# Kernel optimization log

Hardware: AMD Instinct MI355X
Metric: run time of the kernel (lower is better)

Reference implementation:

```python
import jax, jax.numpy as jnp
import numpy as np

NUM_HEADS = 16
THETA = 10000.0


def _rope(x, pos, theta):
    # x: [b, h, s, d_k] with d_k even; rotate interleaved pairs (even, odd)
    d = x.shape[-1]
    inv_freq = theta ** (-jnp.arange(0, d, 2, dtype=jnp.float32) / d)  # [d/2]
    ang = pos.astype(jnp.float32)[:, None] * inv_freq                  # [s, d/2]
    cos = jnp.cos(ang)[None, None]                                     # [1,1,s,d/2]
    sin = jnp.sin(ang)[None, None]
    x1 = x[..., 0::2]
    x2 = x[..., 1::2]
    r1 = x1 * cos - x2 * sin
    r2 = x1 * sin + x2 * cos
    return jnp.stack([r1, r2], axis=-1).reshape(x.shape)


def setup_inputs() -> dict:
    key = jax.random.key(0)
    ks = jax.random.split(key, 5)
    B, S, D = 2, 2048, 1024
    x = jax.random.normal(ks[0], (B, S, D), dtype=jnp.float32)
    scale = 0.02
    Wq = jax.random.normal(ks[1], (D, D), dtype=jnp.float32) * scale
    Wk = jax.random.normal(ks[2], (D, D), dtype=jnp.float32) * scale
    Wv = jax.random.normal(ks[3], (D, D), dtype=jnp.float32) * scale
    Wo = jax.random.normal(ks[4], (D, D), dtype=jnp.float32) * scale
    return {"x": x, "Wq": Wq, "Wk": Wk, "Wv": Wv, "Wo": Wo}


def reference(x, Wq, Wk, Wv, Wo):
    B, S, D = x.shape
    H = NUM_HEADS
    dk = D // H
    # QKV projections (bias-free Linear: y = x @ W^T, W is [out, in])
    q = (x @ Wq.T).reshape(B, S, H, dk).transpose(0, 2, 1, 3)  # [b,h,s,dk]
    k = (x @ Wk.T).reshape(B, S, H, dk).transpose(0, 2, 1, 3)
    v = (x @ Wv.T).reshape(B, S, H, dk).transpose(0, 2, 1, 3)
    pos = jnp.arange(S)
    q = _rope(q, pos, THETA)
    k = _rope(k, pos, THETA)
    # naive masked SDPA, causal mask
    scores = jnp.einsum('bhqd,bhkd->bhqk', q, k) / (dk ** 0.5)
    causal = jnp.tril(jnp.ones((S, S), dtype=bool))
    scores = jnp.where(causal, scores, -jnp.inf)
    attn = jax.nn.softmax(scores, axis=-1)
    out = jnp.einsum('bhqk,bhkd->bhqd', attn, v)
    out = out.transpose(0, 2, 1, 3).reshape(B, S, D)
    return out @ Wo.T
```

## Files before the change

### kernel.cpp

```cpp
#include <hip/hip_runtime.h>
#include <hip/hip_bf16.h>
#include <stdint.h>

typedef __bf16 bf16;
typedef __bf16 bf16x8 __attribute__((ext_vector_type(8)));
typedef float f32x4 __attribute__((ext_vector_type(4)));

#define B_ 2
#define S_ 2048
#define D_ 1024
#define H_ 16
#define DK 64
#define M_ 4096

__device__ __forceinline__ void gload_lds16(const void* g, void* l) {
  __builtin_amdgcn_global_load_lds(
      (const __attribute__((address_space(1))) uint32_t*)(uintptr_t)g,
      (__attribute__((address_space(3))) uint32_t*)(uintptr_t)l, 16, 0, 0);
}

struct alignas(8) B4s { bf16 a, b, c, d; };

__global__ __launch_bounds__(256) void cvt_all_kernel(
    const float* __restrict__ x, const float* __restrict__ wq, const float* __restrict__ wk,
    const float* __restrict__ wv, const float* __restrict__ wo,
    bf16* __restrict__ xb, bf16* __restrict__ wqb, bf16* __restrict__ wkb,
    bf16* __restrict__ wvb, bf16* __restrict__ wob) {
  int i = blockIdx.x * 256 + threadIdx.x;
  const float* src;
  bf16* dst;
  int off;
  if (i < 1048576) { src = x; dst = xb; off = i; }
  else if (i < 1310720) { src = wq; dst = wqb; off = i - 1048576; }
  else if (i < 1572864) { src = wk; dst = wkb; off = i - 1310720; }
  else if (i < 1835008) { src = wv; dst = wvb; off = i - 1572864; }
  else { src = wo; dst = wob; off = i - 1835008; }
  float4 v = reinterpret_cast<const float4*>(src)[off];
  B4s o{(bf16)v.x, (bf16)v.y, (bf16)v.z, (bf16)v.w};
  reinterpret_cast<B4s*>(dst)[off] = o;
}

template <int MODE>
__global__ __launch_bounds__(256) void gemm_kernel(
    const bf16* __restrict__ A,
    const bf16* __restrict__ W0, const bf16* __restrict__ W1, const bf16* __restrict__ W2,
    bf16* __restrict__ q_out, bf16* __restrict__ k_out, bf16* __restrict__ v_out,
    float* __restrict__ c_out) {
  constexpr int BK = 32;
  __shared__ bf16 Alds[128 * BK];
  __shared__ bf16 Blds[128 * BK];
  const int tid = threadIdx.x;
  const int w = tid >> 6, l = tid & 63;
  const int lr = l & 15, lg = l >> 4;
  const int m0 = blockIdx.y * 128;
  const int nt = blockIdx.x;
  const bf16* W;
  int n0;
  if (MODE == 0) {
    W = (nt >> 3) == 0 ? W0 : ((nt >> 3) == 1 ? W1 : W2);
    n0 = (nt & 7) * 128;
  } else {
    W = W0;
    n0 = nt * 128;
  }
  const int K = 1024;
  const int wm = (w >> 1) * 64, wn = (w & 1) * 64;
  const int srow = w * 16 + (l >> 2);
  const int scol = (l & 3) * 8;
  f32x4 acc[4][4] = {};
  for (int k0 = 0; k0 < K; k0 += BK) {
    gload_lds16(A + (size_t)(m0 + srow) * K + k0 + scol, Alds + (w * 16) * BK);
    gload_lds16(A + (size_t)(m0 + 64 + srow) * K + k0 + scol, Alds + (64 + w * 16) * BK);
    gload_lds16(W + (size_t)(n0 + srow) * K + k0 + scol, Blds + (w * 16) * BK);
    gload_lds16(W + (size_t)(n0 + 64 + srow) * K + k0 + scol, Blds + (64 + w * 16) * BK);
    __syncthreads();
    bf16x8 af[4], bfr[4];
#pragma unroll
    for (int f = 0; f < 4; ++f) {
      af[f]  = *reinterpret_cast<const bf16x8*>(Alds + (wm + f * 16 + lr) * BK + lg * 8);
      bfr[f] = *reinterpret_cast<const bf16x8*>(Blds + (wn + f * 16 + lr) * BK + lg * 8);
    }
#pragma unroll
    for (int fm = 0; fm < 4; ++fm)
#pragma unroll
      for (int fn = 0; fn < 4; ++fn)
        acc[fm][fn] = __builtin_amdgcn_mfma_f32_16x16x32_bf16(af[fm], bfr[fn], acc[fm][fn], 0, 0, 0);
    __syncthreads();
  }
#pragma unroll
  for (int fm = 0; fm < 4; ++fm)
#pragma unroll
    for (int fn = 0; fn < 4; ++fn)
#pragma unroll
      for (int r = 0; r < 4; ++r) {
        int m = m0 + wm + fm * 16 + lg * 4 + r;
        int n = n0 + wn + fn * 16 + lr;
        float v = acc[fm][fn][r];
        if (MODE == 0) {
          bf16* dst = (nt >> 3) == 0 ? q_out : ((nt >> 3) == 1 ? k_out : v_out);
          int h = n >> 6, d = n & 63;
          int b = m >> 11, s = m & 2047;
          dst[(((size_t)b * H_ + h) * S_ + s) * DK + d] = (bf16)v;
        } else {
          c_out[(size_t)m * D_ + n] = v;
        }
      }
}

__global__ __launch_bounds__(256) void rope_kernel(bf16* __restrict__ Q, bf16* __restrict__ K) {
  const int NG = 32 * 2048 * 8;
  int idx = blockIdx.x * 256 + threadIdx.x;
  bf16* X = Q;
  float sc = 0.18033688f;
  if (idx >= NG) { X = K; idx -= NG; sc = 1.0f; }
  int g = idx & 7;
  int s = (idx >> 3) & 2047;
  int bh = idx >> 14;
  size_t off = ((size_t)bh * S_ + s) * DK + g * 8;
  bf16x8 v = *reinterpret_cast<const bf16x8*>(X + off);
  bf16x8 o;
  const float c0 = -0.4152410118609203f;
  float fs = (float)s;
#pragma unroll
  for (int p = 0; p < 4; ++p) {
    int i = g * 4 + p;
    float ang = fs * exp2f((float)i * c0);
    float sn = __sinf(ang), cs = __cosf(ang);
    float x1 = (float)v[2 * p], x2 = (float)v[2 * p + 1];
    o[2 * p]     = (bf16)((x1 * cs - x2 * sn) * sc);
    o[2 * p + 1] = (bf16)((x1 * sn + x2 * cs) * sc);
  }
  *reinterpret_cast<bf16x8*>(X + off) = o;
}

__global__ __launch_bounds__(256, 4) void attn_kernel(
    const bf16* __restrict__ Q, const bf16* __restrict__ K, const bf16* __restrict__ V,
    bf16* __restrict__ O) {
  __shared__ bf16 Klds[2][64 * 64];
  __shared__ bf16 Vt[64 * 64];
  __shared__ bf16 Plds[4][16 * 72];
  const int tid = threadIdx.x;
  const int w = tid >> 6, l = tid & 63;
  const int lr = l & 15, lg = l >> 4;
  const int qt = 31 - (int)(blockIdx.x >> 5);
  const int bh = blockIdx.x & 31;
  const size_t base = (size_t)bh * S_ * DK;

  const size_t qoff = base + (size_t)(qt * 64 + w * 16 + lr) * DK;
  bf16x8 qf0 = *reinterpret_cast<const bf16x8*>(Q + qoff + lg * 8);
  bf16x8 qf1 = *reinterpret_cast<const bf16x8*>(Q + qoff + 32 + lg * 8);

  float m_run = -INFINITY, l_run = 0.f;
  f32x4 o_acc[4] = {};
  bf16* Pw = Plds[w];

  const int ksr = l >> 3;
  const int ksc = (l & 7) * 8;

  auto stageK = [&](int kt, int p) {
#pragma unroll
    for (int c2 = 0; c2 < 2; ++c2) {
      int c = w * 2 + c2;
      int row = c * 8 + ksr;
      gload_lds16(K + base + (size_t)(kt * 64 + row) * DK + (ksc ^ ((row & 7) * 8)),
                  &Klds[p][c * 512]);
    }
  };
  auto loadV = [&](int kt, bf16x8& v0, bf16x8& v1) {
    v0 = *reinterpret_cast<const bf16x8*>(V + base + (size_t)(kt * 64 + l) * DK + w * 8);
    v1 = *reinterpret_cast<const bf16x8*>(V + base + (size_t)(kt * 64 + l) * DK + w * 8 + 32);
  };
  auto writeV = [&](const bf16x8& v0, const bf16x8& v1) {
#pragma unroll
    for (int j = 0; j < 8; ++j) {
      Vt[(w * 8 + j) * 64 + (l ^ (j * 8))] = v0[j];
      Vt[(w * 8 + 32 + j) * 64 + (l ^ (j * 8))] = v1[j];
    }
  };

  {
    stageK(0, 0);
    bf16x8 v0, v1;
    loadV(0, v0, v1);
    writeV(v0, v1);
  }
  __syncthreads();

  bf16x8 pv0, pv1;
  for (int kt = 0; kt <= qt; ++kt) {
    const int p = kt & 1;
    const bool pre = kt < qt;
    if (pre) {
      stageK(kt + 1, p ^ 1);
      loadV(kt + 1, pv0, pv1);
    }
    f32x4 s[4];
#pragma unroll
    for (int kf = 0; kf < 4; ++kf) {
      int key = kf * 16 + lr;
      bf16x8 k0 = *reinterpret_cast<const bf16x8*>(
          &Klds[p][key * 64 + ((lg * 8) ^ ((key & 7) * 8))]);
      bf16x8 k1 = *reinterpret_cast<const bf16x8*>(
          &Klds[p][key * 64 + ((32 + lg * 8) ^ ((key & 7) * 8))]);
      f32x4 a = {};
      a = __builtin_amdgcn_mfma_f32_16x16x32_bf16(k0, qf0, a, 0, 0, 0);
      a = __builtin_amdgcn_mfma_f32_16x16x32_bf16(k1, qf1, a, 0, 0, 0);
      s[kf] = a;
    }
    float tmax = -INFINITY;
    const bool lastt = (kt == qt);
#pragma unroll
    for (int kf = 0; kf < 4; ++kf)
#pragma unroll
      for (int r = 0; r < 4; ++r) {
        float v = s[kf][r];
        if (lastt && (kf * 16 + 4 * lg + r > w * 16 + lr)) v = -INFINITY;
        s[kf][r] = v;
        tmax = fmaxf(tmax, v);
      }
    tmax = fmaxf(tmax, __shfl_xor(tmax, 16));
    tmax = fmaxf(tmax, __shfl_xor(tmax, 32));
    if (!__all(tmax <= m_run + 11.0f)) {
      float m_new = fmaxf(m_run, tmax);
      float sf = exp2f(m_run - m_new);
      l_run *= sf;
      float sfr0 = __shfl(sf, 4 * lg + 0);
      float sfr1 = __shfl(sf, 4 * lg + 1);
      float sfr2 = __shfl(sf, 4 * lg + 2);
      float sfr3 = __shfl(sf, 4 * lg + 3);
#pragma unroll
      for (int dt = 0; dt < 4; ++dt) {
        o_acc[dt][0] *= sfr0; o_acc[dt][1] *= sfr1;
        o_acc[dt][2] *= sfr2; o_acc[dt][3] *= sfr3;
      }
      m_run = m_new;
    }
    float ts = 0.f;
#pragma unroll
    for (int kf = 0; kf < 4; ++kf)
#pragma unroll
      for (int r = 0; r < 4; ++r) {
        float pp = exp2f(s[kf][r] - m_run);
        s[kf][r] = pp;
        ts += pp;
      }
    ts += __shfl_xor(ts, 16);
    ts += __shfl_xor(ts, 32);
    l_run += ts;
#pragma unroll
    for (int kf = 0; kf < 4; ++kf) {
      B4s p4{(bf16)s[kf][0], (bf16)s[kf][1], (bf16)s[kf][2], (bf16)s[kf][3]};
      *reinterpret_cast<B4s*>(Pw + lr * 72 + kf * 16 + 4 * lg) = p4;
    }
    bf16x8 pa0 = *reinterpret_cast<const bf16x8*>(Pw + lr * 72 + lg * 8);
    bf16x8 pa1 = *reinterpret_cast<const bf16x8*>(Pw + lr * 72 + 32 + lg * 8);
#pragma unroll
    for (int dt = 0; dt < 4; ++dt) {
      int d = dt * 16 + lr;
      int sw = (d & 7) * 8;
      bf16x8 v0 = *reinterpret_cast<const bf16x8*>(&Vt[d * 64 + ((lg * 8) ^ sw)]);
      bf16x8 v1 = *reinterpret_cast<const bf16x8*>(&Vt[d * 64 + ((32 + lg * 8) ^ sw)]);
      o_acc[dt] = __builtin_amdgcn_mfma_f32_16x16x32_bf16(pa0, v0, o_acc[dt], 0, 0, 0);
      o_acc[dt] = __builtin_amdgcn_mfma_f32_16x16x32_bf16(pa1, v1, o_acc[dt], 0, 0, 0);
    }
    __syncthreads();
    if (pre) writeV(pv0, pv1);
    __syncthreads();
  }

  const int b = bh >> 4, h = bh & 15;
  float inv = 1.0f / l_run;
  float ir[4];
  ir[0] = __shfl(inv, 4 * lg + 0);
  ir[1] = __shfl(inv, 4 * lg + 1);
  ir[2] = __shfl(inv, 4 * lg + 2);
  ir[3] = __shfl(inv, 4 * lg + 3);
#pragma unroll
  for (int dt = 0; dt < 4; ++dt)
#pragma unroll
    for (int r = 0; r < 4; ++r) {
      int qrow = qt * 64 + w * 16 + 4 * lg + r;
      int n = h * DK + dt * 16 + lr;
      O[((size_t)b * S_ + qrow) * D_ + n] = (bf16)(o_acc[dt][r] * ir[r]);
    }
}

extern "C" void kernel_launch(void* const* d_in, const int* in_sizes, int n_in,
                              void* d_out, int out_size, void* d_ws, size_t ws_size,
                              hipStream_t stream) {
  const float* x  = (const float*)d_in[0];
  const float* Wq = (const float*)d_in[1];
  const float* Wk = (const float*)d_in[2];
  const float* Wv = (const float*)d_in[3];
  const float* Wo = (const float*)d_in[4];
  float* out = (float*)d_out;
  char* ws = (char*)d_ws;

  bf16* xb  = (bf16*)(ws + ((size_t)0 << 20));
  bf16* wqb = (bf16*)(ws + ((size_t)8 << 20));
  bf16* wkb = (bf16*)(ws + ((size_t)10 << 20));
  bf16* wvb = (bf16*)(ws + ((size_t)12 << 20));
  bf16* wob = (bf16*)(ws + ((size_t)14 << 20));
  bf16* Qb  = (bf16*)(ws + ((size_t)16 << 20));
  bf16* Kb  = (bf16*)(ws + ((size_t)24 << 20));
  bf16* Vb  = (bf16*)(ws + ((size_t)32 << 20));
  bf16* Ob  = (bf16*)(ws + ((size_t)40 << 20));

  cvt_all_kernel<<<8192, 256, 0, stream>>>(x, Wq, Wk, Wv, Wo, xb, wqb, wkb, wvb, wob);
  gemm_kernel<0><<<dim3(24, 32), 256, 0, stream>>>(xb, wqb, wkb, wvb, Qb, Kb, Vb, nullptr);
  rope_kernel<<<4096, 256, 0, stream>>>(Qb, Kb);
  attn_kernel<<<1024, 256, 0, stream>>>(Qb, Kb, Vb, Ob);
  gemm_kernel<1><<<dim3(8, 32), 256, 0, stream>>>(Ob, wob, nullptr, nullptr, nullptr, nullptr,
                                                  nullptr, out);
}
```

Measured before the change: 127.3 us.

## Restructure attention to 32x32 MFMA with register-resident P and two waves

The attention kernel switches from 16x16x32 MFMA tiles with four waves of 16 query rows to 32x32x16 MFMA tiles with two waves of 32 query rows each. The softmax probabilities are packed into bf16 pairs and redistributed with cross-half lane shuffles instead of a round trip through LDS. The kernel also skips the upper key half on the diagonal tile for the first wave and raises wave priority around the MFMA sections. This aims to cut LDS traffic and instruction count per FLOP, at the cost of fewer threads per block, higher register pressure and a different occupancy profile.

```diff
diff --git a/kernel.cpp b/kernel.cpp
--- a/kernel.cpp
+++ b/kernel.cpp
@@ -5,6 +5,7 @@
 typedef __bf16 bf16;
 typedef __bf16 bf16x8 __attribute__((ext_vector_type(8)));
 typedef float f32x4 __attribute__((ext_vector_type(4)));
+typedef float f32x16 __attribute__((ext_vector_type(16)));
 
 #define B_ 2
 #define S_ 2048
@@ -17,6 +18,12 @@
   __builtin_amdgcn_global_load_lds(
       (const __attribute__((address_space(1))) uint32_t*)(uintptr_t)g,
       (__attribute__((address_space(3))) uint32_t*)(uintptr_t)l, 16, 0, 0);
+}
+
+__device__ __forceinline__ uint32_t pkbf(float a, float b) {
+  union { uint32_t u; struct { bf16 x, y; } s; } r;
+  r.s.x = (bf16)a; r.s.y = (bf16)b;
+  return r.u;
 }
 
 struct alignas(8) B4s { bf16 a, b, c, d; };
@@ -133,156 +140,182 @@
   *reinterpret_cast<bf16x8*>(X + off) = o;
 }
 
-__global__ __launch_bounds__(256, 4) void attn_kernel(
+__global__ __launch_bounds__(128, 2) void attn_kernel(
     const bf16* __restrict__ Q, const bf16* __restrict__ K, const bf16* __restrict__ V,
     bf16* __restrict__ O) {
   __shared__ bf16 Klds[2][64 * 64];
   __shared__ bf16 Vt[64 * 64];
-  __shared__ bf16 Plds[4][16 * 72];
   const int tid = threadIdx.x;
   const int w = tid >> 6, l = tid & 63;
-  const int lr = l & 15, lg = l >> 4;
+  const int ql = l & 31, h = l >> 5;
   const int qt = 31 - (int)(blockIdx.x >> 5);
   const int bh = blockIdx.x & 31;
   const size_t base = (size_t)bh * S_ * DK;
 
-  const size_t qoff = base + (size_t)(qt * 64 + w * 16 + lr) * DK;
-  bf16x8 qf0 = *reinterpret_cast<const bf16x8*>(Q + qoff + lg * 8);
-  bf16x8 qf1 = *reinterpret_cast<const bf16x8*>(Q + qoff + 32 + lg * 8);
+  const size_t qrow = base + (size_t)(qt * 64 + w * 32 + ql) * DK;
+  bf16x8 qf[4];
+#pragma unroll
+  for (int t = 0; t < 4; ++t)
+    qf[t] = *reinterpret_cast<const bf16x8*>(Q + qrow + t * 16 + h * 8);
 
   float m_run = -INFINITY, l_run = 0.f;
-  f32x4 o_acc[4] = {};
-  bf16* Pw = Plds[w];
-
-  const int ksr = l >> 3;
-  const int ksc = (l & 7) * 8;
+  f32x16 o0 = {}, o1 = {};
 
   auto stageK = [&](int kt, int p) {
 #pragma unroll
-    for (int c2 = 0; c2 < 2; ++c2) {
-      int c = w * 2 + c2;
-      int row = c * 8 + ksr;
-      gload_lds16(K + base + (size_t)(kt * 64 + row) * DK + (ksc ^ ((row & 7) * 8)),
-                  &Klds[p][c * 512]);
+    for (int c = 0; c < 4; ++c) {
+      int chunk = c * 128 + tid;
+      int row = chunk >> 3;
+      int colbase = (chunk & 7) * 8;
+      gload_lds16(K + base + (size_t)(kt * 64 + row) * DK + (colbase ^ ((row & 7) * 8)),
+                  &Klds[p][c * 1024 + (tid >> 6) * 512]);
     }
   };
-  auto loadV = [&](int kt, bf16x8& v0, bf16x8& v1) {
-    v0 = *reinterpret_cast<const bf16x8*>(V + base + (size_t)(kt * 64 + l) * DK + w * 8);
-    v1 = *reinterpret_cast<const bf16x8*>(V + base + (size_t)(kt * 64 + l) * DK + w * 8 + 32);
+  const int vkey = tid & 63;
+  const int vdb = (tid >> 6) * 8;
+  auto loadV = [&](int kt, bf16x8 (&pv)[4]) {
+#pragma unroll
+    for (int i = 0; i < 4; ++i)
+      pv[i] = *reinterpret_cast<const bf16x8*>(
+          V + base + (size_t)(kt * 64 + vkey) * DK + vdb + i * 16);
   };
-  auto writeV = [&](const bf16x8& v0, const bf16x8& v1) {
-#pragma unroll
-    for (int j = 0; j < 8; ++j) {
-      Vt[(w * 8 + j) * 64 + (l ^ (j * 8))] = v0[j];
-      Vt[(w * 8 + 32 + j) * 64 + (l ^ (j * 8))] = v1[j];
+  auto writeV = [&](const bf16x8 (&pv)[4]) {
+#pragma unroll
+    for (int i = 0; i < 4; ++i) {
+      int d0 = vdb + i * 16;
+#pragma unroll
+      for (int j = 0; j < 8; ++j)
+        Vt[(d0 + j) * 64 + (vkey ^ (j * 8))] = pv[i][j];
     }
   };
 
   {
     stageK(0, 0);
-    bf16x8 v0, v1;
-    loadV(0, v0, v1);
-    writeV(v0, v1);
+    bf16x8 pv[4];
+    loadV(0, pv);
+    writeV(pv);
   }
   __syncthreads();
 
-  bf16x8 pv0, pv1;
+  const int swzd = (ql & 7) * 8;
+  const int lim = w * 32 + ql;
+  bf16x8 pvv[4];
+
   for (int kt = 0; kt <= qt; ++kt) {
     const int p = kt & 1;
     const bool pre = kt < qt;
+    const bool lastt = (kt == qt);
+    const bool skip1 = lastt && (w == 0);
     if (pre) {
       stageK(kt + 1, p ^ 1);
-      loadV(kt + 1, pv0, pv1);
-    }
-    f32x4 s[4];
-#pragma unroll
-    for (int kf = 0; kf < 4; ++kf) {
-      int key = kf * 16 + lr;
-      bf16x8 k0 = *reinterpret_cast<const bf16x8*>(
-          &Klds[p][key * 64 + ((lg * 8) ^ ((key & 7) * 8))]);
-      bf16x8 k1 = *reinterpret_cast<const bf16x8*>(
-          &Klds[p][key * 64 + ((32 + lg * 8) ^ ((key & 7) * 8))]);
-      f32x4 a = {};
-      a = __builtin_amdgcn_mfma_f32_16x16x32_bf16(k0, qf0, a, 0, 0, 0);
-      a = __builtin_amdgcn_mfma_f32_16x16x32_bf16(k1, qf1, a, 0, 0, 0);
-      s[kf] = a;
+      loadV(kt + 1, pvv);
+    }
+
+    f32x16 ss0 = {}, ss1 = {};
+    __builtin_amdgcn_s_setprio(1);
+#pragma unroll
+    for (int t = 0; t < 4; ++t) {
+      bf16x8 kf = *reinterpret_cast<const bf16x8*>(
+          &Klds[p][ql * 64 + ((t * 16 + h * 8) ^ ((ql & 7) * 8))]);
+      ss0 = __builtin_amdgcn_mfma_f32_32x32x16_bf16(kf, qf[t], ss0, 0, 0, 0);
+    }
+    if (!skip1) {
+#pragma unroll
+      for (int t = 0; t < 4; ++t) {
+        int key = 32 + ql;
+        bf16x8 kf = *reinterpret_cast<const bf16x8*>(
+            &Klds[p][key * 64 + ((t * 16 + h * 8) ^ ((key & 7) * 8))]);
+        ss1 = __builtin_amdgcn_mfma_f32_32x32x16_bf16(kf, qf[t], ss1, 0, 0, 0);
+      }
+    }
+    __builtin_amdgcn_s_setprio(0);
+
+    if (lastt) {
+#pragma unroll
+      for (int r = 0; r < 16; ++r) {
+        int kl = (r & 3) + 8 * (r >> 2) + 4 * h;
+        if (kl > lim) ss0[r] = -INFINITY;
+        if (kl + 32 > lim) ss1[r] = -INFINITY;
+      }
     }
     float tmax = -INFINITY;
-    const bool lastt = (kt == qt);
-#pragma unroll
-    for (int kf = 0; kf < 4; ++kf)
-#pragma unroll
-      for (int r = 0; r < 4; ++r) {
-        float v = s[kf][r];
-        if (lastt && (kf * 16 + 4 * lg + r > w * 16 + lr)) v = -INFINITY;
-        s[kf][r] = v;
-        tmax = fmaxf(tmax, v);
-      }
-    tmax = fmaxf(tmax, __shfl_xor(tmax, 16));
+#pragma unroll
+    for (int r = 0; r < 16; ++r) tmax = fmaxf(tmax, fmaxf(ss0[r], ss1[r]));
     tmax = fmaxf(tmax, __shfl_xor(tmax, 32));
     if (!__all(tmax <= m_run + 11.0f)) {
       float m_new = fmaxf(m_run, tmax);
       float sf = exp2f(m_run - m_new);
       l_run *= sf;
-      float sfr0 = __shfl(sf, 4 * lg + 0);
-      float sfr1 = __shfl(sf, 4 * lg + 1);
-      float sfr2 = __shfl(sf, 4 * lg + 2);
-      float sfr3 = __shfl(sf, 4 * lg + 3);
-#pragma unroll
-      for (int dt = 0; dt < 4; ++dt) {
-        o_acc[dt][0] *= sfr0; o_acc[dt][1] *= sfr1;
-        o_acc[dt][2] *= sfr2; o_acc[dt][3] *= sfr3;
+#pragma unroll
+      for (int r = 0; r < 16; ++r) {
+        float sfr = __shfl(sf, (r & 3) + 8 * (r >> 2) + 4 * h);
+        o0[r] *= sfr;
+        o1[r] *= sfr;
       }
       m_run = m_new;
     }
     float ts = 0.f;
 #pragma unroll
-    for (int kf = 0; kf < 4; ++kf)
-#pragma unroll
-      for (int r = 0; r < 4; ++r) {
-        float pp = exp2f(s[kf][r] - m_run);
-        s[kf][r] = pp;
-        ts += pp;
-      }
-    ts += __shfl_xor(ts, 16);
+    for (int r = 0; r < 16; ++r) {
+      float p0 = exp2f(ss0[r] - m_run);
+      float p1 = exp2f(ss1[r] - m_run);
+      ss0[r] = p0; ss1[r] = p1;
+      ts += p0 + p1;
+    }
     ts += __shfl_xor(ts, 32);
     l_run += ts;
-#pragma unroll
-    for (int kf = 0; kf < 4; ++kf) {
-      B4s p4{(bf16)s[kf][0], (bf16)s[kf][1], (bf16)s[kf][2], (bf16)s[kf][3]};
-      *reinterpret_cast<B4s*>(Pw + lr * 72 + kf * 16 + 4 * lg) = p4;
-    }
-    bf16x8 pa0 = *reinterpret_cast<const bf16x8*>(Pw + lr * 72 + lg * 8);
-    bf16x8 pa1 = *reinterpret_cast<const bf16x8*>(Pw + lr * 72 + 32 + lg * 8);
-#pragma unroll
-    for (int dt = 0; dt < 4; ++dt) {
-      int d = dt * 16 + lr;
-      int sw = (d & 7) * 8;
-      bf16x8 v0 = *reinterpret_cast<const bf16x8*>(&Vt[d * 64 + ((lg * 8) ^ sw)]);
-      bf16x8 v1 = *reinterpret_cast<const bf16x8*>(&Vt[d * 64 + ((32 + lg * 8) ^ sw)]);
-      o_acc[dt] = __builtin_amdgcn_mfma_f32_16x16x32_bf16(pa0, v0, o_acc[dt], 0, 0, 0);
-      o_acc[dt] = __builtin_amdgcn_mfma_f32_16x16x32_bf16(pa1, v1, o_acc[dt], 0, 0, 0);
-    }
+
+    uint32_t W0q[4][2], W1q[4][2];
+#pragma unroll
+    for (int g = 0; g < 4; ++g) {
+      W0q[g][0] = pkbf(ss0[4 * g + 0], ss0[4 * g + 1]);
+      W0q[g][1] = pkbf(ss0[4 * g + 2], ss0[4 * g + 3]);
+      W1q[g][0] = pkbf(ss1[4 * g + 0], ss1[4 * g + 1]);
+      W1q[g][1] = pkbf(ss1[4 * g + 2], ss1[4 * g + 3]);
+    }
+    __builtin_amdgcn_s_setprio(1);
+#pragma unroll
+    for (int t = 0; t < 4; ++t) {
+      if (t >= 2 && skip1) break;
+      const int tt = t & 1;
+      uint32_t a0, a1, b0, b1;
+      if (t < 2) { a0 = W0q[2 * tt][0]; a1 = W0q[2 * tt][1];
+                   b0 = W0q[2 * tt + 1][0]; b1 = W0q[2 * tt + 1][1]; }
+      else       { a0 = W1q[2 * tt][0]; a1 = W1q[2 * tt][1];
+                   b0 = W1q[2 * tt + 1][0]; b1 = W1q[2 * tt + 1][1]; }
+      uint32_t sxa0 = (uint32_t)__shfl_xor((int)a0, 32);
+      uint32_t sxa1 = (uint32_t)__shfl_xor((int)a1, 32);
+      uint32_t sxb0 = (uint32_t)__shfl_xor((int)b0, 32);
+      uint32_t sxb1 = (uint32_t)__shfl_xor((int)b1, 32);
+      union { uint32_t u[4]; bf16x8 v; } pa;
+      pa.u[0] = h ? sxb0 : a0;
+      pa.u[1] = h ? sxb1 : a1;
+      pa.u[2] = h ? b0 : sxa0;
+      pa.u[3] = h ? b1 : sxa1;
+      int col = (t * 16 + h * 8) ^ swzd;
+      bf16x8 v0 = *reinterpret_cast<const bf16x8*>(&Vt[ql * 64 + col]);
+      bf16x8 v1 = *reinterpret_cast<const bf16x8*>(&Vt[(32 + ql) * 64 + col]);
+      o0 = __builtin_amdgcn_mfma_f32_32x32x16_bf16(pa.v, v0, o0, 0, 0, 0);
+      o1 = __builtin_amdgcn_mfma_f32_32x32x16_bf16(pa.v, v1, o1, 0, 0, 0);
+    }
+    __builtin_amdgcn_s_setprio(0);
+
     __syncthreads();
-    if (pre) writeV(pv0, pv1);
+    if (pre) writeV(pvv);
     __syncthreads();
   }
 
-  const int b = bh >> 4, h = bh & 15;
+  const int b = bh >> 4, hd = bh & 15;
   float inv = 1.0f / l_run;
-  float ir[4];
-  ir[0] = __shfl(inv, 4 * lg + 0);
-  ir[1] = __shfl(inv, 4 * lg + 1);
-  ir[2] = __shfl(inv, 4 * lg + 2);
-  ir[3] = __shfl(inv, 4 * lg + 3);
-#pragma unroll
-  for (int dt = 0; dt < 4; ++dt)
-#pragma unroll
-    for (int r = 0; r < 4; ++r) {
-      int qrow = qt * 64 + w * 16 + 4 * lg + r;
-      int n = h * DK + dt * 16 + lr;
-      O[((size_t)b * S_ + qrow) * D_ + n] = (bf16)(o_acc[dt][r] * ir[r]);
-    }
+#pragma unroll
+  for (int r = 0; r < 16; ++r) {
+    int rowl = (r & 3) + 8 * (r >> 2) + 4 * h;
+    float ir = __shfl(inv, rowl);
+    int qr = qt * 64 + w * 32 + rowl;
+    size_t off = ((size_t)b * S_ + qr) * D_ + hd * 64;
+    O[off + ql] = (bf16)(o0[r] * ir);
+    O[off + 32 + ql] = (bf16)(o1[r] * ir);
+  }
 }
 
 extern "C" void kernel_launch(void* const* d_in, const int* in_sizes, int n_in,
@@ -309,7 +342,7 @@
   cvt_all_kernel<<<8192, 256, 0, stream>>>(x, Wq, Wk, Wv, Wo, xb, wqb, wkb, wvb, wob);
   gemm_kernel<0><<<dim3(24, 32), 256, 0, stream>>>(xb, wqb, wkb, wvb, Qb, Kb, Vb, nullptr);
   rope_kernel<<<4096, 256, 0, stream>>>(Qb, Kb);
-  attn_kernel<<<1024, 256, 0, stream>>>(Qb, Kb, Vb, Ob);
+  attn_kernel<<<1024, 128, 0, stream>>>(Qb, Kb, Vb, Ob);
   gemm_kernel<1><<<dim3(8, 32), 256, 0, stream>>>(Ob, wob, nullptr, nullptr, nullptr, nullptr,
                                                   nullptr, out);
 }
```

Measured after the change: 147.4 us. 1.16x slower.
